# Optimization experiments

Hardware: AMD Instinct MI355X
Metric: run time of the kernel (lower is better)

Reference implementation:

```python
import jax, jax.numpy as jnp
import numpy as np

T, V, L, N, D = 4, 2, 3, 4000, 256
TEMP = 0.5


def setup_inputs() -> dict:
    key = jax.random.key(0)
    ks = jax.random.split(key, 9)
    E = jax.random.normal(ks[0], (T, V, L, N, D), dtype=jnp.float32)
    s = 1.0 / np.sqrt(D)
    W1 = jax.random.uniform(ks[1], (D, D), jnp.float32, -s, s)
    b1 = jax.random.uniform(ks[2], (D,), jnp.float32, -s, s)
    W2 = jax.random.uniform(ks[3], (D, D), jnp.float32, -s, s)
    b2 = jax.random.uniform(ks[4], (D,), jnp.float32, -s, s)
    idx_prio = jax.random.randint(ks[5], (2, V, L, 100), 0, N, dtype=jnp.int32)
    idx_rest = jax.random.randint(ks[6], (2, V, L, 20), 0, N, dtype=jnp.int32)
    neg_idx_prio = jax.random.randint(ks[7], (2, V, L, 3, 50), 0, N, dtype=jnp.int32)
    neg_idx_rest = jax.random.randint(ks[8], (2, V, L, 3, 10), 0, N, dtype=jnp.int32)
    return {
        "node_embeddings": E, "W1": W1, "b1": b1, "W2": W2, "b2": b2,
        "idx_prio": idx_prio, "idx_rest": idx_rest,
        "neg_idx_prio": neg_idx_prio, "neg_idx_rest": neg_idx_rest,
        "num_views": 2, "num_layers": 3,
    }


def _proj_norm(x, W1, b1, W2, b2):
    # nn.Linear -> ReLU -> nn.Linear, then F.normalize(p=2, dim=-1)
    h = jax.nn.relu(x @ W1.T + b1)
    z = h @ W2.T + b2
    return z / jnp.maximum(jnp.linalg.norm(z, axis=-1, keepdims=True), 1e-12)


def _type_loss(P, t, idx, nidx):
    # P: [T,V,L,N,D] projected+normalized; idx: [V,L,S] anchor node ids;
    # nidx: [V,L,3,K] cross-type negative node ids (one row per other type).
    vi = jnp.arange(V)[:, None, None]
    li = jnp.arange(L)[None, :, None]
    z = P[t][vi, li, idx]                                  # [V,L,S,D] anchors
    # positives: same node index across every other (view, layer) combo
    Pj = P[t][:, :, idx, :]                                # [X,Y,V,L,S,D]
    sims_pos = jnp.einsum('vlsd,xyvlsd->vlsxy', z, Pj) / TEMP
    same_vl = (jnp.eye(V, dtype=bool)[:, None, :, None]
               & jnp.eye(L, dtype=bool)[None, :, None, :])  # [V,L,X,Y]
    pos = jnp.where(same_vl[:, :, None, :, :], 0.0,
                    jnp.exp(sims_pos)).sum((-2, -1))        # [V,L,S]
    # within-type negatives: the other sampled anchors at the same (v,l)
    S = idx.shape[-1]
    sims_in = jnp.einsum('vlsd,vltd->vlst', z, z) / TEMP
    neg_in = jnp.where(jnp.eye(S, dtype=bool), 0.0,
                       jnp.exp(sims_in)).sum(-1)            # [V,L,S]
    # cross-type negatives: K sampled nodes from each other type at (v,l)
    others = jnp.array([o for o in range(T) if o != t])
    Po = P[others]                                          # [3,V,L,N,D]
    nidx2 = jnp.moveaxis(nidx, 2, 0)                        # [3,V,L,K]
    Pneg = jnp.take_along_axis(Po, nidx2[..., None], axis=3)  # [3,V,L,K,D]
    sims_c = jnp.einsum('vlsd,ovlkd->vlsok', z, Pneg) / TEMP
    neg = neg_in + jnp.exp(sims_c).sum((-2, -1))            # [V,L,S]
    loss = -jnp.log(pos / (pos + neg))
    return loss.sum(), loss.size


def reference(node_embeddings, W1, b1, W2, b2, idx_prio, idx_rest,
              neg_idx_prio, neg_idx_rest, num_views, num_layers):
    P = _proj_norm(node_embeddings, W1, b1, W2, b2)  # [T,V,L,N,D]
    total = jnp.float32(0.0)
    count = 0
    for t in range(T):  # small fixed loop over node types
        if t < 2:
            ls, c = _type_loss(P, t, idx_prio[t], neg_idx_prio[t])
        else:
            ls, c = _type_loss(P, t, idx_rest[t - 2], neg_idx_rest[t - 2])
        total = total + ls
        count += c
    return total / count
```

## Files before the change

kernel.cpp:

```cpp
#include <hip/hip_runtime.h>
#include <math.h>

#define DD 256
#define NV 2
#define NL 3
#define NNODE 4000
#define NROWS_B 8640
#define NROWS 10800
#define NANCH 1440
#define ACC_OFF (10800L * 128)
#define CNT_IDX (ACC_OFF + 2 * NANCH)
#define WP_OFF (ACC_OFF + 2 * NANCH + 4)
#define XPAD 260
#define NTASK 2136
#define NBLK_SIM (NTASK / 4)

typedef __attribute__((ext_vector_type(8))) short short8;
typedef __attribute__((ext_vector_type(4))) short short4v;
typedef __attribute__((ext_vector_type(4))) float f32x4;

__device__ __forceinline__ unsigned short f2bf(float f) {
  unsigned u = __float_as_uint(f);
  u += 0x7fff + ((u >> 16) & 1);
  return (unsigned short)(u >> 16);
}

__device__ __forceinline__ int tb_B(int t) { return (t < 2) ? t * 3600 : 7200 + (t - 2) * 720; }
__device__ __forceinline__ int tb_C(int t) { return (t < 2) ? t * 900 : 1800 + (t - 2) * 180; }
__device__ __forceinline__ int anch_base(int t, int vl) {
  return ((t < 2) ? t * 600 : 1200 + (t - 2) * 120) + vl * ((t < 2) ? 100 : 20);
}

__device__ __forceinline__ long row_src(int u, const int* __restrict__ ip,
                                        const int* __restrict__ ir,
                                        const int* __restrict__ npg,
                                        const int* __restrict__ nrg) {
  int t, x, y, node;
  if (u < NROWS_B) {
    int S, u2;
    if (u < 7200) { t = u / 3600; u2 = u - t * 3600; S = 100; }
    else { int w = u - 7200; t = 2 + w / 720; u2 = w % 720; S = 20; }
    int s = u2 % S; int t1 = u2 / S;
    int l = t1 % NL; int t2 = t1 / NL;
    int v = t2 % NV; int xy = t2 / NV;
    x = xy / NL; y = xy % NL;
    if (t < 2) node = ip[((t * NV + v) * NL + l) * 100 + s];
    else       node = ir[(((t - 2) * NV + v) * NL + l) * 20 + s];
  } else {
    int w = u - NROWS_B;
    int K, u2;
    if (w < 1800) { t = w / 900; u2 = w % 900; K = 50; }
    else { int w2 = w - 1800; t = 2 + w2 / 180; u2 = w2 % 180; K = 10; }
    int k = u2 % K; int t1 = u2 / K;
    int l = t1 % NL; int t2 = t1 / NL;
    int v = t2 % NV; int o = t2 / NV;
    if (t < 2) node = npg[(((t * NV + v) * NL + l) * 3 + o) * 50 + k];
    else       node = nrg[((((t - 2) * NV + v) * NL + l) * 3 + o) * 10 + k];
    int ot = (o < t) ? o : o + 1;
    t = ot; x = v; y = l;
  }
  return ((((long)t * NV + x) * NL + y) * NNODE + node) * DD;
}

__global__ __launch_bounds__(256) void k_prep(const float* __restrict__ W1,
                                              const float* __restrict__ W2,
                                              float* __restrict__ ws) {
  int tid = blockIdx.x * 256 + threadIdx.x;
  if (tid < 2 * NANCH + 4) ws[ACC_OFF + tid] = 0.0f;
  int st = tid >> 13, rem = tid & 8191;
  int cg = rem >> 9, kstep = (rem >> 6) & 7, lane = rem & 63;
  const float* W = st ? W2 : W1;
  int col = cg * 16 + (lane & 15);
  int k0 = kstep * 32 + (lane >> 4) * 8;
  unsigned short v[8] __attribute__((aligned(16)));
#pragma unroll
  for (int j = 0; j < 8; ++j) v[j] = f2bf(W[col * DD + k0 + j]);
  unsigned short* wp = (unsigned short*)(ws + WP_OFF);
  *(uint4*)(wp + (long)tid * 8) = *(const uint4*)v;
}

__global__ __launch_bounds__(256) void k_proj(const float* __restrict__ E,
                                              const float* __restrict__ b1,
                                              const float* __restrict__ b2,
                                              const int* __restrict__ ip,
                                              const int* __restrict__ ir,
                                              const int* __restrict__ npg,
                                              const int* __restrict__ nrg,
                                              float* __restrict__ ws) {
  __shared__ unsigned short Xs[16][XPAD];
  __shared__ unsigned short Hs[16][XPAD];
  __shared__ float ssbuf[4][16];
  const int tid = threadIdx.x;
  const int u0 = blockIdx.x * 16;
  const int wv = tid >> 6, l64 = tid & 63;
  const int quad = l64 >> 4, l15 = l64 & 15;
  const int cb = wv * 64;
  const unsigned short* wp = (const unsigned short*)(ws + WP_OFF);
  unsigned short* zb = (unsigned short*)ws;

  for (int i = 0; i < 4; ++i) {
    int r = wv * 4 + i;
    int u = u0 + r;
    long src = row_src(u, ip, ir, npg, nrg);
    float4 val = *(const float4*)(E + src + l64 * 4);
    unsigned short h[4] __attribute__((aligned(8)));
    h[0] = f2bf(val.x); h[1] = f2bf(val.y); h[2] = f2bf(val.z); h[3] = f2bf(val.w);
    *(uint2*)(&Xs[r][l64 * 4]) = *(const uint2*)h;
  }

  f32x4 acc[4];
#pragma unroll
  for (int cg = 0; cg < 4; ++cg) {
    float bv = b1[cb + cg * 16 + l15];
    acc[cg] = (f32x4){bv, bv, bv, bv};
  }
  __syncthreads();
#pragma unroll
  for (int ks = 0; ks < 8; ++ks) {
    const unsigned short* ap = &Xs[l15][ks * 32 + quad * 8];
    short4v alo = *(const short4v*)(ap);
    short4v ahi = *(const short4v*)(ap + 4);
    short8 a = __builtin_shufflevector(alo, ahi, 0, 1, 2, 3, 4, 5, 6, 7);
#pragma unroll
    for (int cg = 0; cg < 4; ++cg) {
      short8 b = *(const short8*)(wp + ((long)(((wv * 4 + cg) * 8 + ks) * 64 + l64)) * 8);
      acc[cg] = __builtin_amdgcn_mfma_f32_16x16x32_bf16(a, b, acc[cg], 0, 0, 0);
    }
  }
  __syncthreads();
#pragma unroll
  for (int cg = 0; cg < 4; ++cg) {
    int col = cb + cg * 16 + l15;
#pragma unroll
    for (int reg = 0; reg < 4; ++reg) {
      int row = quad * 4 + reg;
      Hs[row][col] = f2bf(fmaxf(acc[cg][reg], 0.0f));
    }
  }
#pragma unroll
  for (int cg = 0; cg < 4; ++cg) {
    float bv = b2[cb + cg * 16 + l15];
    acc[cg] = (f32x4){bv, bv, bv, bv};
  }
  __syncthreads();
#pragma unroll
  for (int ks = 0; ks < 8; ++ks) {
    const unsigned short* ap = &Hs[l15][ks * 32 + quad * 8];
    short4v alo = *(const short4v*)(ap);
    short4v ahi = *(const short4v*)(ap + 4);
    short8 a = __builtin_shufflevector(alo, ahi, 0, 1, 2, 3, 4, 5, 6, 7);
#pragma unroll
    for (int cg = 0; cg < 4; ++cg) {
      short8 b = *(const short8*)(wp + ((long)((16 + wv * 4 + cg) * 8 + ks) * 64 + l64) * 8);
      acc[cg] = __builtin_amdgcn_mfma_f32_16x16x32_bf16(a, b, acc[cg], 0, 0, 0);
    }
  }
  float ss[4];
#pragma unroll
  for (int reg = 0; reg < 4; ++reg) {
    float s = 0.f;
#pragma unroll
    for (int cg = 0; cg < 4; ++cg) s = fmaf(acc[cg][reg], acc[cg][reg], s);
    ss[reg] = s;
  }
#pragma unroll
  for (int m = 1; m < 16; m <<= 1) {
#pragma unroll
    for (int reg = 0; reg < 4; ++reg) ss[reg] += __shfl_xor(ss[reg], m, 64);
  }
  if (l15 == 0) {
#pragma unroll
    for (int reg = 0; reg < 4; ++reg) ssbuf[wv][quad * 4 + reg] = ss[reg];
  }
  __syncthreads();
#pragma unroll
  for (int reg = 0; reg < 4; ++reg) {
    int row = quad * 4 + reg;
    int u = u0 + row;
    float tot = ssbuf[0][row] + ssbuf[1][row] + ssbuf[2][row] + ssbuf[3][row];
    float sc = 1.0f / fmaxf(sqrtf(tot), 1e-12f);
#pragma unroll
    for (int cg = 0; cg < 4; ++cg)
      zb[(long)u * DD + cb + cg * 16 + l15] = f2bf(acc[cg][reg] * sc);
  }
}

__global__ __launch_bounds__(256) void k_sim(float* __restrict__ ws,
                                             float* __restrict__ out) {
  __shared__ float red[256];
  __shared__ int lastFlag;
  const unsigned short* zb = (const unsigned short*)ws;
  float* posG = ws + ACC_OFF;
  float* negG = ws + ACC_OFF + NANCH;
  int* cnt = (int*)(ws + CNT_IDX);

  const int tid = threadIdx.x;
  const int wv = tid >> 6, l64 = tid & 63;
  const int quad = l64 >> 4, l15 = l64 & 15;
  const int task = blockIdx.x * 4 + wv;

  int t, vl, mt, c;
  if (task < 2016) { t = task / 1008; int r = task % 1008;
                     vl = r / 168; int r2 = r % 168; mt = r2 / 24; c = r2 % 24; }
  else { int q = task - 2016; t = 2 + q / 60; int r2 = q % 60;
         vl = r2 / 10; int r3 = r2 % 10; mt = r3 / 5; c = r3 % 5; }
  const int v = vl / NL, l = vl % NL;
  const int S = (t < 2) ? 100 : 20, K = (t < 2) ? 50 : 10;
  const int Ptot = 6 * S + 3 * K;
  const int ab = anch_base(t, vl);
  const int rowZbase = tb_B(t) + ((vl * NV + v) * NL + l) * S;

  int am = mt * 16 + l15;
  int amc = (am < S) ? am : (S - 1);
  const unsigned short* abase = zb + (long)(rowZbase + amc) * DD + quad * 8;
  short8 afr[8];
#pragma unroll
  for (int ks = 0; ks < 8; ++ks) afr[ks] = *(const short8*)(abase + ks * 32);

  float negAcc[4] = {0.f, 0.f, 0.f, 0.f};
#pragma unroll
  for (int nt = 0; nt < 2; ++nt) {
    int qg = c * 32 + nt * 16 + l15;
    bool vq = (qg < Ptot);
    int qc = vq ? qg : 0;
    int rowb, xy = -1, j = -1;
    if (qc < 6 * S) {
      xy = qc / S; j = qc - xy * S;
      rowb = tb_B(t) + ((xy * NV + v) * NL + l) * S + j;
    } else {
      int q2 = qc - 6 * S; int o = q2 / K, k2 = q2 - o * K;
      rowb = NROWS_B + tb_C(t) + ((o * NV + v) * NL + l) * K + k2;
    }
    const unsigned short* bbase = zb + (long)rowb * DD + quad * 8;
    f32x4 acc = {0.f, 0.f, 0.f, 0.f};
#pragma unroll
    for (int ks = 0; ks < 8; ++ks) {
      short8 bfr = *(const short8*)(bbase + ks * 32);
      acc = __builtin_amdgcn_mfma_f32_16x16x32_bf16(afr[ks], bfr, acc, 0, 0, 0);
    }
#pragma unroll
    for (int r = 0; r < 4; ++r) {
      int a = mt * 16 + quad * 4 + r;
      if (!vq || a >= S) continue;
      float e = expf(2.0f * acc[r]);
      if (xy >= 0) {
        if (xy == vl) { if (j != a) negAcc[r] += e; }
        else if (j == a) atomicAdd(&posG[ab + a], e);
      } else {
        negAcc[r] += e;
      }
    }
  }
#pragma unroll
  for (int m = 1; m < 16; m <<= 1) {
#pragma unroll
    for (int r = 0; r < 4; ++r) negAcc[r] += __shfl_xor(negAcc[r], m, 64);
  }
  if (l15 == 0) {
#pragma unroll
    for (int r = 0; r < 4; ++r) {
      int a = mt * 16 + quad * 4 + r;
      if (a < S) atomicAdd(&negG[ab + a], negAcc[r]);
    }
  }
  __threadfence();
  __syncthreads();
  if (tid == 0) {
    int old = atomicAdd(cnt, 1);
    lastFlag = (old == NBLK_SIM - 1) ? 1 : 0;
  }
  __syncthreads();
  if (lastFlag) {
    float sum = 0.f;
    for (int i = tid; i < NANCH; i += 256) {
      float p = atomicAdd(&posG[i], 0.0f);
      float n = atomicAdd(&negG[i], 0.0f);
      sum += -logf(p / (p + n));
    }
    red[tid] = sum;
    __syncthreads();
    for (int s = 128; s > 0; s >>= 1) {
      if (tid < s) red[tid] += red[tid + s];
      __syncthreads();
    }
    if (tid == 0) out[0] = red[0] / (float)NANCH;
  }
}

extern "C" void kernel_launch(void* const* d_in, const int* in_sizes, int n_in,
                              void* d_out, int out_size, void* d_ws, size_t ws_size,
                              hipStream_t stream) {
  const float* E  = (const float*)d_in[0];
  const float* W1 = (const float*)d_in[1];
  const float* b1 = (const float*)d_in[2];
  const float* W2 = (const float*)d_in[3];
  const float* b2 = (const float*)d_in[4];
  const int* ip  = (const int*)d_in[5];
  const int* ir  = (const int*)d_in[6];
  const int* npg = (const int*)d_in[7];
  const int* nrg = (const int*)d_in[8];
  float* ws = (float*)d_ws;
  float* out = (float*)d_out;

  hipLaunchKernelGGL(k_prep, dim3(64), dim3(256), 0, stream, W1, W2, ws);
  hipLaunchKernelGGL(k_proj, dim3(NROWS / 16), dim3(256), 0, stream,
                     E, b1, b2, ip, ir, npg, nrg, ws);
  hipLaunchKernelGGL(k_sim, dim3(NBLK_SIM), dim3(256), 0, stream, ws, out);
}
```

Baseline: 203.2 us.

## Process 32 rows per projection block, reorder packed weights, stagger k-steps

```diff
diff --git a/kernel.cpp b/kernel.cpp
--- a/kernel.cpp
+++ b/kernel.cpp
@@ -11,12 +11,11 @@
 #define ACC_OFF (10800L * 128)
 #define CNT_IDX (ACC_OFF + 2 * NANCH)
 #define WP_OFF (ACC_OFF + 2 * NANCH + 4)
-#define XPAD 260
+#define XPAD 264
 #define NTASK 2136
 #define NBLK_SIM (NTASK / 4)
 
 typedef __attribute__((ext_vector_type(8))) short short8;
-typedef __attribute__((ext_vector_type(4))) short short4v;
 typedef __attribute__((ext_vector_type(4))) float f32x4;
 
 __device__ __forceinline__ unsigned short f2bf(float f) {
@@ -67,11 +66,10 @@
                                               float* __restrict__ ws) {
   int tid = blockIdx.x * 256 + threadIdx.x;
   if (tid < 2 * NANCH + 4) ws[ACC_OFF + tid] = 0.0f;
-  int st = tid >> 13, rem = tid & 8191;
-  int cg = rem >> 9, kstep = (rem >> 6) & 7, lane = rem & 63;
+  int st = tid >> 13, ks = (tid >> 10) & 7, cgg = (tid >> 6) & 15, lane = tid & 63;
   const float* W = st ? W2 : W1;
-  int col = cg * 16 + (lane & 15);
-  int k0 = kstep * 32 + (lane >> 4) * 8;
+  int col = cgg * 16 + (lane & 15);
+  int k0 = ks * 32 + (lane >> 4) * 8;
   unsigned short v[8] __attribute__((aligned(16)));
 #pragma unroll
   for (int j = 0; j < 8; ++j) v[j] = f2bf(W[col * DD + k0 + j]);
@@ -87,102 +85,122 @@
                                               const int* __restrict__ npg,
                                               const int* __restrict__ nrg,
                                               float* __restrict__ ws) {
-  __shared__ unsigned short Xs[16][XPAD];
-  __shared__ unsigned short Hs[16][XPAD];
-  __shared__ float ssbuf[4][16];
+  __shared__ unsigned short Xs[32][XPAD];
+  __shared__ unsigned short Hs[32][XPAD];
+  __shared__ float ssbuf[4][32];
   const int tid = threadIdx.x;
-  const int u0 = blockIdx.x * 16;
+  const int bid = blockIdx.x;
+  const int u0 = bid * 32;
   const int wv = tid >> 6, l64 = tid & 63;
   const int quad = l64 >> 4, l15 = l64 & 15;
   const int cb = wv * 64;
   const unsigned short* wp = (const unsigned short*)(ws + WP_OFF);
   unsigned short* zb = (unsigned short*)ws;
 
-  for (int i = 0; i < 4; ++i) {
-    int r = wv * 4 + i;
+  for (int i = 0; i < 8; ++i) {
+    int r = wv * 8 + i;
     int u = u0 + r;
-    long src = row_src(u, ip, ir, npg, nrg);
-    float4 val = *(const float4*)(E + src + l64 * 4);
+    float4 val = make_float4(0.f, 0.f, 0.f, 0.f);
+    if (u < NROWS) {
+      long src = row_src(u, ip, ir, npg, nrg);
+      val = *(const float4*)(E + src + l64 * 4);
+    }
     unsigned short h[4] __attribute__((aligned(8)));
     h[0] = f2bf(val.x); h[1] = f2bf(val.y); h[2] = f2bf(val.z); h[3] = f2bf(val.w);
     *(uint2*)(&Xs[r][l64 * 4]) = *(const uint2*)h;
   }
 
-  f32x4 acc[4];
+  f32x4 acc[4][2];
 #pragma unroll
   for (int cg = 0; cg < 4; ++cg) {
     float bv = b1[cb + cg * 16 + l15];
-    acc[cg] = (f32x4){bv, bv, bv, bv};
-  }
-  __syncthreads();
-#pragma unroll
-  for (int ks = 0; ks < 8; ++ks) {
-    const unsigned short* ap = &Xs[l15][ks * 32 + quad * 8];
-    short4v alo = *(const short4v*)(ap);
-    short4v ahi = *(const short4v*)(ap + 4);
-    short8 a = __builtin_shufflevector(alo, ahi, 0, 1, 2, 3, 4, 5, 6, 7);
-#pragma unroll
-    for (int cg = 0; cg < 4; ++cg) {
-      short8 b = *(const short8*)(wp + ((long)(((wv * 4 + cg) * 8 + ks) * 64 + l64)) * 8);
-      acc[cg] = __builtin_amdgcn_mfma_f32_16x16x32_bf16(a, b, acc[cg], 0, 0, 0);
-    }
-  }
-  __syncthreads();
+    acc[cg][0] = (f32x4){bv, bv, bv, bv};
+    acc[cg][1] = (f32x4){bv, bv, bv, bv};
+  }
+  __syncthreads();
+#pragma unroll
+  for (int ks0 = 0; ks0 < 8; ++ks0) {
+    int ks = (ks0 + bid) & 7;
+    short8 a0 = *(const short8*)(&Xs[l15][ks * 32 + quad * 8]);
+    short8 a1 = *(const short8*)(&Xs[16 + l15][ks * 32 + quad * 8]);
+#pragma unroll
+    for (int cg0 = 0; cg0 < 4; ++cg0) {
+      int cg = (cg0 + bid) & 3;
+      int cgg = wv * 4 + cg;
+      short8 b = *(const short8*)(wp + ((long)((ks * 16 + cgg) * 64 + l64)) * 8);
+      acc[cg][0] = __builtin_amdgcn_mfma_f32_16x16x32_bf16(a0, b, acc[cg][0], 0, 0, 0);
+      acc[cg][1] = __builtin_amdgcn_mfma_f32_16x16x32_bf16(a1, b, acc[cg][1], 0, 0, 0);
+    }
+  }
 #pragma unroll
   for (int cg = 0; cg < 4; ++cg) {
     int col = cb + cg * 16 + l15;
 #pragma unroll
-    for (int reg = 0; reg < 4; ++reg) {
-      int row = quad * 4 + reg;
-      Hs[row][col] = f2bf(fmaxf(acc[cg][reg], 0.0f));
-    }
+    for (int mt = 0; mt < 2; ++mt)
+#pragma unroll
+      for (int reg = 0; reg < 4; ++reg)
+        Hs[mt * 16 + quad * 4 + reg][col] = f2bf(fmaxf(acc[cg][mt][reg], 0.0f));
   }
 #pragma unroll
   for (int cg = 0; cg < 4; ++cg) {
     float bv = b2[cb + cg * 16 + l15];
-    acc[cg] = (f32x4){bv, bv, bv, bv};
-  }
-  __syncthreads();
-#pragma unroll
-  for (int ks = 0; ks < 8; ++ks) {
-    const unsigned short* ap = &Hs[l15][ks * 32 + quad * 8];
-    short4v alo = *(const short4v*)(ap);
-    short4v ahi = *(const short4v*)(ap + 4);
-    short8 a = __builtin_shufflevector(alo, ahi, 0, 1, 2, 3, 4, 5, 6, 7);
-#pragma unroll
-    for (int cg = 0; cg < 4; ++cg) {
-      short8 b = *(const short8*)(wp + ((long)((16 + wv * 4 + cg) * 8 + ks) * 64 + l64) * 8);
-      acc[cg] = __builtin_amdgcn_mfma_f32_16x16x32_bf16(a, b, acc[cg], 0, 0, 0);
-    }
-  }
-  float ss[4];
-#pragma unroll
-  for (int reg = 0; reg < 4; ++reg) {
-    float s = 0.f;
-#pragma unroll
-    for (int cg = 0; cg < 4; ++cg) s = fmaf(acc[cg][reg], acc[cg][reg], s);
-    ss[reg] = s;
-  }
+    acc[cg][0] = (f32x4){bv, bv, bv, bv};
+    acc[cg][1] = (f32x4){bv, bv, bv, bv};
+  }
+  __syncthreads();
+#pragma unroll
+  for (int ks0 = 0; ks0 < 8; ++ks0) {
+    int ks = (ks0 + bid) & 7;
+    short8 a0 = *(const short8*)(&Hs[l15][ks * 32 + quad * 8]);
+    short8 a1 = *(const short8*)(&Hs[16 + l15][ks * 32 + quad * 8]);
+#pragma unroll
+    for (int cg0 = 0; cg0 < 4; ++cg0) {
+      int cg = (cg0 + bid) & 3;
+      int cgg = wv * 4 + cg;
+      short8 b = *(const short8*)(wp + ((long)(((8 + ks) * 16 + cgg) * 64 + l64)) * 8);
+      acc[cg][0] = __builtin_amdgcn_mfma_f32_16x16x32_bf16(a0, b, acc[cg][0], 0, 0, 0);
+      acc[cg][1] = __builtin_amdgcn_mfma_f32_16x16x32_bf16(a1, b, acc[cg][1], 0, 0, 0);
+    }
+  }
+  float ss[2][4];
+#pragma unroll
+  for (int mt = 0; mt < 2; ++mt)
+#pragma unroll
+    for (int reg = 0; reg < 4; ++reg) {
+      float s = 0.f;
+#pragma unroll
+      for (int cg = 0; cg < 4; ++cg) s = fmaf(acc[cg][mt][reg], acc[cg][mt][reg], s);
+      ss[mt][reg] = s;
+    }
 #pragma unroll
   for (int m = 1; m < 16; m <<= 1) {
 #pragma unroll
-    for (int reg = 0; reg < 4; ++reg) ss[reg] += __shfl_xor(ss[reg], m, 64);
+    for (int mt = 0; mt < 2; ++mt)
+#pragma unroll
+      for (int reg = 0; reg < 4; ++reg) ss[mt][reg] += __shfl_xor(ss[mt][reg], m, 64);
   }
   if (l15 == 0) {
 #pragma unroll
-    for (int reg = 0; reg < 4; ++reg) ssbuf[wv][quad * 4 + reg] = ss[reg];
-  }
-  __syncthreads();
-#pragma unroll
-  for (int reg = 0; reg < 4; ++reg) {
-    int row = quad * 4 + reg;
-    int u = u0 + row;
-    float tot = ssbuf[0][row] + ssbuf[1][row] + ssbuf[2][row] + ssbuf[3][row];
-    float sc = 1.0f / fmaxf(sqrtf(tot), 1e-12f);
-#pragma unroll
-    for (int cg = 0; cg < 4; ++cg)
-      zb[(long)u * DD + cb + cg * 16 + l15] = f2bf(acc[cg][reg] * sc);
-  }
+    for (int mt = 0; mt < 2; ++mt)
+#pragma unroll
+      for (int reg = 0; reg < 4; ++reg)
+        ssbuf[wv][mt * 16 + quad * 4 + reg] = ss[mt][reg];
+  }
+  __syncthreads();
+#pragma unroll
+  for (int mt = 0; mt < 2; ++mt)
+#pragma unroll
+    for (int reg = 0; reg < 4; ++reg) {
+      int row = mt * 16 + quad * 4 + reg;
+      int u = u0 + row;
+      if (u < NROWS) {
+        float tot = ssbuf[0][row] + ssbuf[1][row] + ssbuf[2][row] + ssbuf[3][row];
+        float sc = 1.0f / fmaxf(sqrtf(tot), 1e-12f);
+#pragma unroll
+        for (int cg = 0; cg < 4; ++cg)
+          zb[(long)u * DD + cb + cg * 16 + l15] = f2bf(acc[cg][mt][reg] * sc);
+      }
+    }
 }
 
 __global__ __launch_bounds__(256) void k_sim(float* __restrict__ ws,
@@ -303,7 +321,7 @@
   float* out = (float*)d_out;
 
   hipLaunchKernelGGL(k_prep, dim3(64), dim3(256), 0, stream, W1, W2, ws);
-  hipLaunchKernelGGL(k_proj, dim3(NROWS / 16), dim3(256), 0, stream,
+  hipLaunchKernelGGL(k_proj, dim3((NROWS + 31) / 32), dim3(256), 0, stream,
                      E, b1, b2, ip, ir, npg, nrg, ws);
   hipLaunchKernelGGL(k_sim, dim3(NBLK_SIM), dim3(256), 0, stream, ws, out);
 }
```

Result: slower. 225.8 us (+11.1%).

## Make projection kernel persistent with register-resident weight fragments

Applied to the files above, without the earlier changes.

```diff
diff --git a/kernel.cpp b/kernel.cpp
--- a/kernel.cpp
+++ b/kernel.cpp
@@ -11,12 +11,12 @@
 #define ACC_OFF (10800L * 128)
 #define CNT_IDX (ACC_OFF + 2 * NANCH)
 #define WP_OFF (ACC_OFF + 2 * NANCH + 4)
-#define XPAD 260
+#define XPAD 264
 #define NTASK 2136
 #define NBLK_SIM (NTASK / 4)
+#define NBLK_PROJ 225
 
 typedef __attribute__((ext_vector_type(8))) short short8;
-typedef __attribute__((ext_vector_type(4))) short short4v;
 typedef __attribute__((ext_vector_type(4))) float f32x4;
 
 __device__ __forceinline__ unsigned short f2bf(float f) {
@@ -67,11 +67,10 @@
                                               float* __restrict__ ws) {
   int tid = blockIdx.x * 256 + threadIdx.x;
   if (tid < 2 * NANCH + 4) ws[ACC_OFF + tid] = 0.0f;
-  int st = tid >> 13, rem = tid & 8191;
-  int cg = rem >> 9, kstep = (rem >> 6) & 7, lane = rem & 63;
+  int st = tid >> 13, ks = (tid >> 10) & 7, cgg = (tid >> 6) & 15, lane = tid & 63;
   const float* W = st ? W2 : W1;
-  int col = cg * 16 + (lane & 15);
-  int k0 = kstep * 32 + (lane >> 4) * 8;
+  int col = cgg * 16 + (lane & 15);
+  int k0 = ks * 32 + (lane >> 4) * 8;
   unsigned short v[8] __attribute__((aligned(16)));
 #pragma unroll
   for (int j = 0; j < 8; ++j) v[j] = f2bf(W[col * DD + k0 + j]);
@@ -79,109 +78,111 @@
   *(uint4*)(wp + (long)tid * 8) = *(const uint4*)v;
 }
 
-__global__ __launch_bounds__(256) void k_proj(const float* __restrict__ E,
-                                              const float* __restrict__ b1,
-                                              const float* __restrict__ b2,
-                                              const int* __restrict__ ip,
-                                              const int* __restrict__ ir,
-                                              const int* __restrict__ npg,
-                                              const int* __restrict__ nrg,
-                                              float* __restrict__ ws) {
+__global__ __launch_bounds__(512, 2) void k_proj(const float* __restrict__ E,
+                                                 const float* __restrict__ b1,
+                                                 const float* __restrict__ b2,
+                                                 const int* __restrict__ ip,
+                                                 const int* __restrict__ ir,
+                                                 const int* __restrict__ npg,
+                                                 const int* __restrict__ nrg,
+                                                 float* __restrict__ ws) {
   __shared__ unsigned short Xs[16][XPAD];
   __shared__ unsigned short Hs[16][XPAD];
-  __shared__ float ssbuf[4][16];
+  __shared__ float ssbuf[8][16];
   const int tid = threadIdx.x;
-  const int u0 = blockIdx.x * 16;
   const int wv = tid >> 6, l64 = tid & 63;
   const int quad = l64 >> 4, l15 = l64 & 15;
-  const int cb = wv * 64;
+  const int cb = wv * 32;
   const unsigned short* wp = (const unsigned short*)(ws + WP_OFF);
   unsigned short* zb = (unsigned short*)ws;
 
-  for (int i = 0; i < 4; ++i) {
-    int r = wv * 4 + i;
-    int u = u0 + r;
-    long src = row_src(u, ip, ir, npg, nrg);
-    float4 val = *(const float4*)(E + src + l64 * 4);
-    unsigned short h[4] __attribute__((aligned(8)));
-    h[0] = f2bf(val.x); h[1] = f2bf(val.y); h[2] = f2bf(val.z); h[3] = f2bf(val.w);
-    *(uint2*)(&Xs[r][l64 * 4]) = *(const uint2*)h;
-  }
-
-  f32x4 acc[4];
-#pragma unroll
-  for (int cg = 0; cg < 4; ++cg) {
-    float bv = b1[cb + cg * 16 + l15];
-    acc[cg] = (f32x4){bv, bv, bv, bv};
-  }
-  __syncthreads();
-#pragma unroll
-  for (int ks = 0; ks < 8; ++ks) {
-    const unsigned short* ap = &Xs[l15][ks * 32 + quad * 8];
-    short4v alo = *(const short4v*)(ap);
-    short4v ahi = *(const short4v*)(ap + 4);
-    short8 a = __builtin_shufflevector(alo, ahi, 0, 1, 2, 3, 4, 5, 6, 7);
-#pragma unroll
-    for (int cg = 0; cg < 4; ++cg) {
-      short8 b = *(const short8*)(wp + ((long)(((wv * 4 + cg) * 8 + ks) * 64 + l64)) * 8);
-      acc[cg] = __builtin_amdgcn_mfma_f32_16x16x32_bf16(a, b, acc[cg], 0, 0, 0);
-    }
-  }
-  __syncthreads();
-#pragma unroll
-  for (int cg = 0; cg < 4; ++cg) {
-    int col = cb + cg * 16 + l15;
+  short8 bfr[2][8][2];
+#pragma unroll
+  for (int st = 0; st < 2; ++st)
+#pragma unroll
+    for (int ks = 0; ks < 8; ++ks)
+#pragma unroll
+      for (int cg = 0; cg < 2; ++cg)
+        bfr[st][ks][cg] = *(const short8*)(
+            wp + ((long)(((st * 8 + ks) * 16 + (wv * 2 + cg)) * 64 + l64)) * 8);
+
+  float bv1[2], bv2[2];
+#pragma unroll
+  for (int cg = 0; cg < 2; ++cg) {
+    bv1[cg] = b1[cb + cg * 16 + l15];
+    bv2[cg] = b2[cb + cg * 16 + l15];
+  }
+
+  for (int it = 0; it < 3; ++it) {
+    int rt = blockIdx.x + it * NBLK_PROJ;
+    int u0 = rt * 16;
+
+#pragma unroll
+    for (int i = 0; i < 2; ++i) {
+      int r = wv * 2 + i;
+      long src = row_src(u0 + r, ip, ir, npg, nrg);
+      float4 val = *(const float4*)(E + src + l64 * 4);
+      unsigned short h[4] __attribute__((aligned(8)));
+      h[0] = f2bf(val.x); h[1] = f2bf(val.y); h[2] = f2bf(val.z); h[3] = f2bf(val.w);
+      *(uint2*)(&Xs[r][l64 * 4]) = *(const uint2*)h;
+    }
+    __syncthreads();
+
+    f32x4 acc[2];
+#pragma unroll
+    for (int cg = 0; cg < 2; ++cg) acc[cg] = (f32x4){bv1[cg], bv1[cg], bv1[cg], bv1[cg]};
+#pragma unroll
+    for (int ks = 0; ks < 8; ++ks) {
+      short8 a = *(const short8*)(&Xs[l15][ks * 32 + quad * 8]);
+#pragma unroll
+      for (int cg = 0; cg < 2; ++cg)
+        acc[cg] = __builtin_amdgcn_mfma_f32_16x16x32_bf16(a, bfr[0][ks][cg], acc[cg], 0, 0, 0);
+    }
+#pragma unroll
+    for (int cg = 0; cg < 2; ++cg) {
+      int col = cb + cg * 16 + l15;
+#pragma unroll
+      for (int reg = 0; reg < 4; ++reg)
+        Hs[quad * 4 + reg][col] = f2bf(fmaxf(acc[cg][reg], 0.0f));
+    }
+    __syncthreads();
+
+#pragma unroll
+    for (int cg = 0; cg < 2; ++cg) acc[cg] = (f32x4){bv2[cg], bv2[cg], bv2[cg], bv2[cg]};
+#pragma unroll
+    for (int ks = 0; ks < 8; ++ks) {
+      short8 a = *(const short8*)(&Hs[l15][ks * 32 + quad * 8]);
+#pragma unroll
+      for (int cg = 0; cg < 2; ++cg)
+        acc[cg] = __builtin_amdgcn_mfma_f32_16x16x32_bf16(a, bfr[1][ks][cg], acc[cg], 0, 0, 0);
+    }
+
+    float ss[4];
+#pragma unroll
+    for (int reg = 0; reg < 4; ++reg)
+      ss[reg] = fmaf(acc[0][reg], acc[0][reg], acc[1][reg] * acc[1][reg]);
+#pragma unroll
+    for (int m = 1; m < 16; m <<= 1) {
+#pragma unroll
+      for (int reg = 0; reg < 4; ++reg) ss[reg] += __shfl_xor(ss[reg], m, 64);
+    }
+    if (l15 == 0) {
+#pragma unroll
+      for (int reg = 0; reg < 4; ++reg) ssbuf[wv][quad * 4 + reg] = ss[reg];
+    }
+    __syncthreads();
 #pragma unroll
     for (int reg = 0; reg < 4; ++reg) {
       int row = quad * 4 + reg;
-      Hs[row][col] = f2bf(fmaxf(acc[cg][reg], 0.0f));
-    }
-  }
-#pragma unroll
-  for (int cg = 0; cg < 4; ++cg) {
-    float bv = b2[cb + cg * 16 + l15];
-    acc[cg] = (f32x4){bv, bv, bv, bv};
-  }
-  __syncthreads();
-#pragma unroll
-  for (int ks = 0; ks < 8; ++ks) {
-    const unsigned short* ap = &Hs[l15][ks * 32 + quad * 8];
-    short4v alo = *(const short4v*)(ap);
-    short4v ahi = *(const short4v*)(ap + 4);
-    short8 a = __builtin_shufflevector(alo, ahi, 0, 1, 2, 3, 4, 5, 6, 7);
-#pragma unroll
-    for (int cg = 0; cg < 4; ++cg) {
-      short8 b = *(const short8*)(wp + ((long)((16 + wv * 4 + cg) * 8 + ks) * 64 + l64) * 8);
-      acc[cg] = __builtin_amdgcn_mfma_f32_16x16x32_bf16(a, b, acc[cg], 0, 0, 0);
-    }
-  }
-  float ss[4];
-#pragma unroll
-  for (int reg = 0; reg < 4; ++reg) {
-    float s = 0.f;
-#pragma unroll
-    for (int cg = 0; cg < 4; ++cg) s = fmaf(acc[cg][reg], acc[cg][reg], s);
-    ss[reg] = s;
-  }
-#pragma unroll
-  for (int m = 1; m < 16; m <<= 1) {
-#pragma unroll
-    for (int reg = 0; reg < 4; ++reg) ss[reg] += __shfl_xor(ss[reg], m, 64);
-  }
-  if (l15 == 0) {
-#pragma unroll
-    for (int reg = 0; reg < 4; ++reg) ssbuf[wv][quad * 4 + reg] = ss[reg];
-  }
-  __syncthreads();
-#pragma unroll
-  for (int reg = 0; reg < 4; ++reg) {
-    int row = quad * 4 + reg;
-    int u = u0 + row;
-    float tot = ssbuf[0][row] + ssbuf[1][row] + ssbuf[2][row] + ssbuf[3][row];
-    float sc = 1.0f / fmaxf(sqrtf(tot), 1e-12f);
-#pragma unroll
-    for (int cg = 0; cg < 4; ++cg)
-      zb[(long)u * DD + cb + cg * 16 + l15] = f2bf(acc[cg][reg] * sc);
+      float tot = 0.f;
+#pragma unroll
+      for (int w2 = 0; w2 < 8; ++w2) tot += ssbuf[w2][row];
+      float sc = 1.0f / fmaxf(sqrtf(tot), 1e-12f);
+#pragma unroll
+      for (int cg = 0; cg < 2; ++cg)
+        zb[(long)(u0 + row) * DD + cb + cg * 16 + l15] = f2bf(acc[cg][reg] * sc);
+    }
+    __syncthreads();
   }
 }
 
@@ -235,8 +236,8 @@
     f32x4 acc = {0.f, 0.f, 0.f, 0.f};
 #pragma unroll
     for (int ks = 0; ks < 8; ++ks) {
-      short8 bfr = *(const short8*)(bbase + ks * 32);
-      acc = __builtin_amdgcn_mfma_f32_16x16x32_bf16(afr[ks], bfr, acc, 0, 0, 0);
+      short8 bfr2 = *(const short8*)(bbase + ks * 32);
+      acc = __builtin_amdgcn_mfma_f32_16x16x32_bf16(afr[ks], bfr2, acc, 0, 0, 0);
     }
 #pragma unroll
     for (int r = 0; r < 4; ++r) {
@@ -303,7 +304,7 @@
   float* out = (float*)d_out;
 
   hipLaunchKernelGGL(k_prep, dim3(64), dim3(256), 0, stream, W1, W2, ws);
-  hipLaunchKernelGGL(k_proj, dim3(NROWS / 16), dim3(256), 0, stream,
+  hipLaunchKernelGGL(k_proj, dim3(NBLK_PROJ), dim3(512), 0, stream,
                      E, b1, b2, ip, ir, npg, nrg, ws);
   hipLaunchKernelGGL(k_sim, dim3(NBLK_SIM), dim3(256), 0, stream, ws, out);
 }
```

Result: no change. 205.4 us (+1.1%).
